# Performance work log

Measured on AMD Instinct MI355X. Metric: run time of the kernel, lower is better.

## Reference

```python
import jax, jax.numpy as jnp
import numpy as np

B, S, D, H, F = 4, 1024, 1024, 16, 4096
DH = D // H
EPS = 1e-3  # keras LayerNormalization default epsilon


def _layer_norm(x, g, b):
    mu = jnp.mean(x, axis=-1, keepdims=True)
    var = jnp.mean(jnp.square(x - mu), axis=-1, keepdims=True)
    return (x - mu) * jax.lax.rsqrt(var + EPS) * g + b


def setup_inputs() -> dict:
    key = jax.random.key(0)
    ks = jax.random.split(key, 12)
    p = lambda k, shape: (0.02 * jax.random.normal(k, shape, dtype=jnp.float32))
    inp = {
        "inputs": jax.random.normal(ks[0], (B, S, D), dtype=jnp.float32),
        "paddings": jnp.zeros((B, S), dtype=jnp.float32),
        "attention_bias": jax.random.normal(ks[1], (B, H, S, S), dtype=jnp.float32),
        "attention_mask": jnp.ones((B, S, S), dtype=jnp.float32),
        "ln1_g": jnp.ones((D,), jnp.float32), "ln1_b": jnp.zeros((D,), jnp.float32),
        "wq": p(ks[2], (D, D)), "bq": jnp.zeros((D,), jnp.float32),
        "wk": p(ks[3], (D, D)), "bk": jnp.zeros((D,), jnp.float32),
        "wv": p(ks[4], (D, D)), "bv": jnp.zeros((D,), jnp.float32),
        "wo": p(ks[5], (D, D)), "bo": jnp.zeros((D,), jnp.float32),
        "ln2_g": jnp.ones((D,), jnp.float32), "ln2_b": jnp.zeros((D,), jnp.float32),
        "w1": p(ks[6], (D, F)), "b1": jnp.zeros((F,), jnp.float32),
        "w2": p(ks[7], (F, D)), "b2": jnp.zeros((D,), jnp.float32),
    }
    return inp


def reference(inputs, paddings, attention_bias, attention_mask,
              ln1_g, ln1_b, wq, bq, wk, bk, wv, bv, wo, bo,
              ln2_g, ln2_b, w1, b1, w2, b2):
    # ----- combined mask: [B,S,S] (broadcast over heads) -----
    keep = 1.0 - paddings                           # [B,S]
    pad_mask = keep[:, :, None] * keep[:, None, :]  # [B,T,S]
    mask = attention_mask * pad_mask                # [B,T,S]

    # ----- self-attention on pre-normalized inputs -----
    xn = _layer_norm(inputs, ln1_g, ln1_b)          # [B,S,D]
    q = (xn @ wq + bq).reshape(B, S, H, DH)
    k = (xn @ wk + bk).reshape(B, S, H, DH)
    v = (xn @ wv + bv).reshape(B, S, H, DH)

    logits = jnp.einsum('bthd,bshd->bhts', q, k) / jnp.sqrt(jnp.float32(DH))
    logits = logits + attention_bias - 1e9 * (1.0 - mask[:, None, :, :])
    attn = jax.nn.softmax(logits, axis=-1)          # [B,H,T,S]
    ctx = jnp.einsum('bhts,bshd->bthd', attn, v).reshape(B, S, D)
    atten_out = ctx @ wo + bo + inputs              # residual

    # ----- feed-forward block -----
    yn = _layer_norm(atten_out, ln2_g, ln2_b)
    h = jax.nn.gelu(yn @ w1 + b1, approximate=False)  # keras 'gelu' is exact
    out = atten_out + (h @ w2 + b2)
    out = out * (1.0 - paddings[:, :, None])
    return out
```

## Files before the change

kernel.cpp:

```cpp
#include <hip/hip_runtime.h>
#include <cstdint>
#include <cstddef>

#define B_   4
#define S_   1024
#define D_   1024
#define H_   16
#define DH_  64
#define F_   4096
#define MTOT 4096
#define QKV3 3072
#define KOFF 1024
#define VOFF 2048
#define SMBASE 16.0f

typedef __bf16 bf16x8 __attribute__((ext_vector_type(8)));
typedef float  f32x4  __attribute__((ext_vector_type(4)));

__device__ __forceinline__ unsigned short f2bf(float f){
  uint32_t u = __builtin_bit_cast(uint32_t, f);
  u += 0x7fffu + ((u >> 16) & 1u);
  return (unsigned short)(u >> 16);
}

__device__ __forceinline__ void gload_lds16(const void* g, void* l){
  __builtin_amdgcn_global_load_lds((__attribute__((address_space(1))) void*)(g),
                                   (__attribute__((address_space(3))) void*)(l),
                                   16, 0, 0);
}

__global__ __launch_bounds__(256) void prep_weights(const float* __restrict__ wq,
                                                    const float* __restrict__ wk,
                                                    const float* __restrict__ wv,
                                                    const float* __restrict__ wo,
                                                    const float* __restrict__ w1,
                                                    const float* __restrict__ w2,
                                                    const float* __restrict__ bq,
                                                    const float* __restrict__ bk,
                                                    const float* __restrict__ bv,
                                                    unsigned short* __restrict__ wqkvT,
                                                    unsigned short* __restrict__ woT,
                                                    unsigned short* __restrict__ w1T,
                                                    unsigned short* __restrict__ w2T,
                                                    float* __restrict__ bqkv){
  __shared__ float tile[32][33];
  const int bid = blockIdx.x;
  const int tx = threadIdx.x, ty = threadIdx.y;
  const float* W; unsigned short* WT; int K, N, n0, k0;
  if (bid < 3072){
    W  = (bid < 1024) ? wq : (bid < 2048) ? wk : wv;
    WT = wqkvT + (size_t)(bid >> 10) * D_ * D_;
    K = D_; N = D_;
    const int t = bid & 1023; n0 = (t & 31) * 32; k0 = (t >> 5) * 32;
  } else if (bid < 4096){
    W = wo; WT = woT; K = D_; N = D_;
    const int t = bid - 3072; n0 = (t & 31) * 32; k0 = (t >> 5) * 32;
  } else if (bid < 8192){
    W = w1; WT = w1T; K = D_; N = F_;
    const int t = bid - 4096; n0 = (t & 127) * 32; k0 = (t >> 7) * 32;
  } else {
    W = w2; WT = w2T; K = F_; N = D_;
    const int t = bid - 8192; n0 = (t & 31) * 32; k0 = (t >> 5) * 32;
  }
  #pragma unroll
  for (int i = 0; i < 4; ++i)
    tile[ty + i*8][tx] = W[(size_t)(k0 + ty + i*8) * N + n0 + tx];
  __syncthreads();
  #pragma unroll
  for (int i = 0; i < 4; ++i)
    WT[(size_t)(n0 + ty + i*8) * K + k0 + tx] = f2bf(tile[tx][ty + i*8]);
  if (bid < 12){
    const int i = bid*256 + ty*32 + tx;
    bqkv[i] = (i < 1024) ? bq[i] : (i < 2048) ? bk[i - 1024] : bv[i - 2048];
  }
}

__global__ __launch_bounds__(256) void vtrans(const unsigned short* __restrict__ qkv,
                                              unsigned short* __restrict__ vt){
  __shared__ unsigned short tile[32][33];
  const int tx = threadIdx.x, ty = threadIdx.y;
  const int bid = blockIdx.x;
  const int s0 = (bid & 31) * 32;
  const int d0 = ((bid >> 5) & 1) * 32;
  const int bh = bid >> 6;
  const int b = bh >> 4, hh = bh & 15;
  #pragma unroll
  for (int i = 0; i < 4; ++i)
    tile[ty + i*8][tx] = qkv[(size_t)(b*S_ + s0 + ty + i*8) * QKV3 + VOFF + hh*DH_ + d0 + tx];
  __syncthreads();
  #pragma unroll
  for (int i = 0; i < 4; ++i)
    vt[((size_t)bh*DH_ + d0 + ty + i*8) * S_ + s0 + tx] = tile[tx][ty + i*8];
}

__global__ __launch_bounds__(256) void ln_kernel(const float* __restrict__ x,
                                                 const float* __restrict__ g,
                                                 const float* __restrict__ b,
                                                 unsigned short* __restrict__ out){
  const int row = blockIdx.x;
  const int tid = threadIdx.x;
  float4 xv = ((const float4*)(x + (size_t)row * D_))[tid];
  float s  = xv.x + xv.y + xv.z + xv.w;
  float s2 = xv.x*xv.x + xv.y*xv.y + xv.z*xv.z + xv.w*xv.w;
  #pragma unroll
  for (int off = 32; off > 0; off >>= 1){
    s  += __shfl_down(s, off);
    s2 += __shfl_down(s2, off);
  }
  __shared__ float ws1[4], ws2[4];
  const int w = tid >> 6, lane = tid & 63;
  if (lane == 0){ ws1[w] = s; ws2[w] = s2; }
  __syncthreads();
  const float tot  = ws1[0] + ws1[1] + ws1[2] + ws1[3];
  const float tot2 = ws2[0] + ws2[1] + ws2[2] + ws2[3];
  const float mean = tot * (1.0f / D_);
  const float var  = tot2 * (1.0f / D_) - mean * mean;
  const float rstd = rsqrtf(var + 1e-3f);
  const int c0 = tid * 4;
  ushort4 o;
  o.x = f2bf((xv.x - mean) * rstd * g[c0+0] + b[c0+0]);
  o.y = f2bf((xv.y - mean) * rstd * g[c0+1] + b[c0+1]);
  o.z = f2bf((xv.z - mean) * rstd * g[c0+2] + b[c0+2]);
  o.w = f2bf((xv.w - mean) * rstd * g[c0+3] + b[c0+3]);
  *(ushort4*)(out + (size_t)row * D_ + c0) = o;
}

template<int EPI, int BM>
__global__ __launch_bounds__(256) void gemm_bt(const unsigned short* __restrict__ A,
                                               const unsigned short* __restrict__ BT,
                                               const float* __restrict__ bias,
                                               const float* __restrict__ resid,
                                               const float* __restrict__ pad,
                                               unsigned short* __restrict__ outB,
                                               float* __restrict__ outF,
                                               int N, int K){
  constexpr int MR = BM / 32;
  constexpr int RA = BM / 32;
  __shared__ unsigned short As[BM * 64];
  __shared__ unsigned short Bs[128 * 64];
  const int tid  = threadIdx.x;
  const int lane = tid & 63, w = tid >> 6;
  const int wr = w >> 1, wc = w & 1;
  const int lm = lane & 15, l4 = lane >> 4;
  const int xsw = (lm & 7) << 3;
  const int m0 = blockIdx.x * BM, n0 = blockIdx.y * 128;

  const int rrow = tid >> 3;
  const int ce   = (((tid & 7) ^ (rrow & 7)) << 3);
  const unsigned short* Asrc = A  + (size_t)(m0 + rrow) * K + ce;
  const unsigned short* Bsrc = BT + (size_t)(n0 + rrow) * K + ce;

  f32x4 acc[MR][4] = {};

  #pragma unroll
  for (int ra = 0; ra < RA; ++ra)
    gload_lds16(Asrc + (size_t)(ra*32) * K, &As[(ra*256 + w*64) * 8]);
  #pragma unroll
  for (int rb = 0; rb < 4; ++rb)
    gload_lds16(Bsrc + (size_t)(rb*32) * K, &Bs[(rb*256 + w*64) * 8]);

  for (int k0 = 0; k0 < K; k0 += 64){
    __syncthreads();

    bf16x8 a[MR][2], bb[4][2];
    #pragma unroll
    for (int m = 0; m < MR; ++m)
      #pragma unroll
      for (int kc = 0; kc < 2; ++kc)
        a[m][kc] = *(const bf16x8*)&As[(wr*(BM/2) + m*16 + lm)*64 + ((kc*32 + l4*8) ^ xsw)];
    #pragma unroll
    for (int n = 0; n < 4; ++n)
      #pragma unroll
      for (int kc = 0; kc < 2; ++kc)
        bb[n][kc] = *(const bf16x8*)&Bs[(wc*64 + n*16 + lm)*64 + ((kc*32 + l4*8) ^ xsw)];

    __syncthreads();

    if (k0 + 64 < K){
      #pragma unroll
      for (int ra = 0; ra < RA; ++ra)
        gload_lds16(Asrc + (size_t)(ra*32) * K + (k0 + 64), &As[(ra*256 + w*64) * 8]);
      #pragma unroll
      for (int rb = 0; rb < 4; ++rb)
        gload_lds16(Bsrc + (size_t)(rb*32) * K + (k0 + 64), &Bs[(rb*256 + w*64) * 8]);
    }

    #pragma unroll
    for (int m = 0; m < MR; ++m)
      #pragma unroll
      for (int n = 0; n < 4; ++n)
        #pragma unroll
        for (int kc = 0; kc < 2; ++kc)
          acc[m][n] = __builtin_amdgcn_mfma_f32_16x16x32_bf16(a[m][kc], bb[n][kc], acc[m][n], 0, 0, 0);
  }

  #pragma unroll
  for (int m = 0; m < MR; ++m){
    #pragma unroll
    for (int n = 0; n < 4; ++n){
      #pragma unroll
      for (int r = 0; r < 4; ++r){
        const int row = m0 + wr*(BM/2) + m*16 + l4*4 + r;
        const int col = n0 + wc*64 + n*16 + lm;
        const size_t idx = (size_t)row * N + col;
        float vv = acc[m][n][r] + bias[col];
        if constexpr (EPI == 0){
          outB[idx] = f2bf(vv);
        } else if constexpr (EPI == 1){
          outF[idx] = vv + resid[idx];
        } else if constexpr (EPI == 2){
          outB[idx] = f2bf(0.5f * vv * (1.0f + erff(vv * 0.70710678118654752f)));
        } else {
          float t = vv + resid[idx];
          outF[idx] = t * (1.0f - pad[row]);
        }
      }
    }
  }
}

__global__ __launch_bounds__(256) void attn_kernel(const unsigned short* __restrict__ qkv,
                                                   const unsigned short* __restrict__ vt,
                                                   const float* __restrict__ abias,
                                                   const float* __restrict__ amask,
                                                   const float* __restrict__ pad,
                                                   unsigned short* __restrict__ ctx){
  const int bid = blockIdx.x;
  const int id2 = (bid & 7) * 128 + (bid >> 3);
  const int tt = id2 & 15, h = (id2 >> 4) & 15, b = id2 >> 8;
  const int t0 = tt * 64;
  const int tid = threadIdx.x;
  const int lane = tid & 63, w = tid >> 6;
  const int lm = lane & 15, l4 = lane >> 4;
  const int xsw = (lm & 7) << 3;

  __shared__ unsigned short Ks[2][64 * 64];
  __shared__ unsigned short VTs[2][64 * 64];
  __shared__ unsigned short Ps[4][16 * 64];

  bf16x8 aq[2];
  {
    const int tg = t0 + w*16 + lm;
    const size_t qb = (size_t)(b*S_ + tg) * QKV3 + h*DH_;
    aq[0] = *(const bf16x8*)&qkv[qb + 0  + l4*8];
    aq[1] = *(const bf16x8*)&qkv[qb + 32 + l4*8];
  }

  const unsigned short* kbase = qkv + (size_t)(b*S_) * QKV3 + KOFF + h*DH_;
  const unsigned short* vbase = vt  + (size_t)((b*H_ + h) * DH_) * S_;
  const float* biasbase  = abias + (size_t)((b*H_ + h) * S_ + t0 + w*16 + l4*4) * S_;
  const float* amaskbase = amask + (size_t)(b*S_ + t0 + w*16 + l4*4) * S_;
  const float* padb = pad + b*S_;

  const int r_st  = tid >> 3;
  const int ce_st = (((tid & 7) ^ (r_st & 7)) << 3);
  const unsigned short* kst = kbase + (size_t)r_st * QKV3 + ce_st;
  const unsigned short* vst = vbase + (size_t)r_st * S_ + ce_st;

  float kt[4];
  #pragma unroll
  for (int r = 0; r < 4; ++r)
    kt[r] = 1.0f - padb[t0 + w*16 + l4*4 + r];

  f32x4 accO[4] = {};
  float lrow[4] = {};
  float bmA[4][4], bmB[4][4];
  float mmA[4][4], mmB[4][4];
  float ksA[4],    ksB[4];

  auto stageKV = [&](int s0, int buf){
    gload_lds16(kst + (size_t)s0*QKV3,        &Ks[buf][w*512]);
    gload_lds16(kst + (size_t)(s0 + 32)*QKV3, &Ks[buf][2048 + w*512]);
    gload_lds16(vst + s0,                     &VTs[buf][w*512]);
    gload_lds16(vst + 32*S_ + s0,             &VTs[buf][2048 + w*512]);
  };
  auto fetchScal = [&](int s0, float (&bm)[4][4], float (&mm)[4][4], float (&ks)[4]){
    #pragma unroll
    for (int n = 0; n < 4; ++n){
      const int sg = s0 + n*16 + lm;
      ks[n] = 1.0f - padb[sg];
      #pragma unroll
      for (int r = 0; r < 4; ++r){
        bm[n][r] = biasbase[(size_t)r * S_ + sg];
        mm[n][r] = amaskbase[(size_t)r * S_ + sg];
      }
    }
  };

  stageKV(0, 0);
  fetchScal(0, bmA, mmA, ksA);

  auto step = [&](int s0, int buf, float (&bm)[4][4], float (&mm)[4][4], float (&ks)[4],
                  float (&bmN)[4][4], float (&mmN)[4][4], float (&ksN)[4]){
    __syncthreads();

    const int s1 = s0 + 64;
    if (s1 < S_){
      stageKV(s1, buf^1);
      fetchScal(s1, bmN, mmN, ksN);
    }

    f32x4 accS[4] = {};
    __builtin_amdgcn_s_setprio(1);
    #pragma unroll
    for (int n = 0; n < 4; ++n)
      #pragma unroll
      for (int kc = 0; kc < 2; ++kc){
        bf16x8 bk_ = *(const bf16x8*)&Ks[buf][(n*16 + lm)*64 + ((kc*32 + l4*8) ^ xsw)];
        accS[n] = __builtin_amdgcn_mfma_f32_16x16x32_bf16(aq[kc], bk_, accS[n], 0, 0, 0);
      }
    __builtin_amdgcn_s_setprio(0);

    float ps[4] = {};
    #pragma unroll
    for (int n = 0; n < 4; ++n){
      #pragma unroll
      for (int r = 0; r < 4; ++r){
        const float mmv = mm[n][r] * kt[r] * ks[n];
        const float ma  = -1e9f * (1.0f - mmv);
        const float pv  = __expf(fmaf(accS[n][r], 0.125f, bm[n][r] + ma) - SMBASE);
        accS[n][r] = pv;
        ps[r] += pv;
      }
    }
    #pragma unroll
    for (int r = 0; r < 4; ++r){
      float s = ps[r];
      s += __shfl_xor(s, 1); s += __shfl_xor(s, 2);
      s += __shfl_xor(s, 4); s += __shfl_xor(s, 8);
      lrow[r] += s;
    }

    #pragma unroll
    for (int n = 0; n < 4; ++n)
      #pragma unroll
      for (int r = 0; r < 4; ++r){
        const int prow = l4*4 + r;
        Ps[w][prow*64 + ((n*16 + lm) ^ ((prow & 7) << 3))] = f2bf(accS[n][r]);
      }

    __builtin_amdgcn_s_setprio(1);
    #pragma unroll
    for (int ks2 = 0; ks2 < 2; ++ks2){
      bf16x8 ap = *(const bf16x8*)&Ps[w][lm*64 + ((ks2*32 + l4*8) ^ xsw)];
      #pragma unroll
      for (int n = 0; n < 4; ++n){
        bf16x8 bv_ = *(const bf16x8*)&VTs[buf][(n*16 + lm)*64 + ((ks2*32 + l4*8) ^ xsw)];
        accO[n] = __builtin_amdgcn_mfma_f32_16x16x32_bf16(ap, bv_, accO[n], 0, 0, 0);
      }
    }
    __builtin_amdgcn_s_setprio(0);
  };

  #pragma unroll 1
  for (int s0 = 0; s0 < S_; s0 += 128){
    step(s0,      0, bmA, mmA, ksA, bmB, mmB, ksB);
    step(s0 + 64, 1, bmB, mmB, ksB, bmA, mmA, ksA);
  }

  #pragma unroll
  for (int n = 0; n < 4; ++n)
    #pragma unroll
    for (int r = 0; r < 4; ++r){
      const int tg = t0 + w*16 + l4*4 + r;
      ctx[(size_t)(b*S_ + tg) * D_ + h*DH_ + n*16 + lm] = f2bf(accO[n][r] / lrow[r]);
    }
}

extern "C" void kernel_launch(void* const* d_in, const int* in_sizes, int n_in,
                              void* d_out, int out_size, void* d_ws, size_t ws_size,
                              hipStream_t stream){
  (void)in_sizes; (void)n_in; (void)out_size; (void)ws_size;
  const float* x     = (const float*)d_in[0];
  const float* pad   = (const float*)d_in[1];
  const float* abias = (const float*)d_in[2];
  const float* amask = (const float*)d_in[3];
  const float* ln1g  = (const float*)d_in[4];
  const float* ln1b  = (const float*)d_in[5];
  const float* wq    = (const float*)d_in[6];
  const float* bq    = (const float*)d_in[7];
  const float* wk    = (const float*)d_in[8];
  const float* bk    = (const float*)d_in[9];
  const float* wv    = (const float*)d_in[10];
  const float* bv    = (const float*)d_in[11];
  const float* wo    = (const float*)d_in[12];
  const float* bo    = (const float*)d_in[13];
  const float* ln2g  = (const float*)d_in[14];
  const float* ln2b  = (const float*)d_in[15];
  const float* w1    = (const float*)d_in[16];
  const float* b1    = (const float*)d_in[17];
  const float* w2    = (const float*)d_in[18];
  const float* b2    = (const float*)d_in[19];
  float* out = (float*)d_out;

  char* p = (char*)d_ws;
  auto take = [&](size_t bytes){ void* r = (void*)p; p += bytes; return r; };
  unsigned short* xn   = (unsigned short*)take((size_t)MTOT * D_ * 2);
  unsigned short* qkv  = (unsigned short*)take((size_t)MTOT * QKV3 * 2);
  unsigned short* ctx  = (unsigned short*)take((size_t)MTOT * D_ * 2);
  unsigned short* yn   = (unsigned short*)take((size_t)MTOT * D_ * 2);
  unsigned short* hb   = (unsigned short*)take((size_t)MTOT * F_ * 2);
  float*          ao   = (float*)take((size_t)MTOT * D_ * 4);
  unsigned short* wqkvT= (unsigned short*)take((size_t)QKV3 * D_ * 2);
  unsigned short* woT  = (unsigned short*)take((size_t)D_ * D_ * 2);
  unsigned short* w1T  = (unsigned short*)take((size_t)D_ * F_ * 2);
  unsigned short* w2T  = (unsigned short*)take((size_t)D_ * F_ * 2);
  float*          bqkv = (float*)take((size_t)QKV3 * 4);
  unsigned short* vtb  = xn;

  const dim3 tb(32, 8);

  prep_weights<<<12288, tb, 0, stream>>>(wq, wk, wv, wo, w1, w2, bq, bk, bv,
                                         wqkvT, woT, w1T, w2T, bqkv);

  ln_kernel<<<MTOT, 256, 0, stream>>>(x, ln1g, ln1b, xn);

  gemm_bt<0,128><<<dim3(MTOT/128, QKV3/128), 256, 0, stream>>>(xn, wqkvT, bqkv, nullptr, nullptr, qkv, nullptr, QKV3, D_);

  vtrans<<<4096, tb, 0, stream>>>(qkv, vtb);

  attn_kernel<<<dim3(16*H_*B_), 256, 0, stream>>>(qkv, vtb, abias, amask, pad, ctx);

  gemm_bt<1,64><<<dim3(MTOT/64, D_/128), 256, 0, stream>>>(ctx, woT, bo, x, nullptr, nullptr, ao, D_, D_);

  ln_kernel<<<MTOT, 256, 0, stream>>>(ao, ln2g, ln2b, yn);

  gemm_bt<2,128><<<dim3(MTOT/128, F_/128), 256, 0, stream>>>(yn, w1T, b1, nullptr, nullptr, hb, nullptr, F_, D_);

  gemm_bt<3,64><<<dim3(MTOT/64, D_/128), 256, 0, stream>>>(hb, w2T, b2, ao, pad, nullptr, out, D_, F_);
}
```

Measured before the change: 306.6 us.

## Add 256x256-tile 8-wave GEMM with interleaved LDS staging for QKV and FFN1

Adds a new 512-thread GEMM kernel with 256x256 output tiles, double-buffered LDS split into k-halves, and a ping-pong schedule that interleaves async global-to-LDS loads with MFMA blocks separated by barriers and priority hints. The QKV projection and the first FFN GEMM now use it instead of the 128-tile kernel. The larger tile raises arithmetic intensity and data reuse per block, and the interleaving hides load latency. In exchange, the grid gets smaller (192 and 256 blocks) and register pressure rises from the 8x4 accumulator array.

```diff
diff --git a/kernel.cpp b/kernel.cpp
--- a/kernel.cpp
+++ b/kernel.cpp
@@ -219,6 +219,145 @@
   }
 }
 
+template<int EPI>
+__global__ __launch_bounds__(512, 2) void gemm8(const unsigned short* __restrict__ A,
+                                                const unsigned short* __restrict__ BT,
+                                                const float* __restrict__ bias,
+                                                unsigned short* __restrict__ outB,
+                                                int N, int K){
+  __shared__ unsigned short As[2][2][256 * 32];
+  __shared__ unsigned short Bs[2][2][256 * 32];
+  const int tid  = threadIdx.x;
+  const int lane = tid & 63, w = tid >> 6;
+  const int wr = w >> 2, wn = w & 3;
+  const int lm = lane & 15, l4 = lane >> 4;
+  const int m0 = blockIdx.x * 256, n0 = blockIdx.y * 256;
+  const int nt = K >> 6;
+
+  const int p_line = tid >> 3, p_c = tid & 7;
+  const int cp     = p_c ^ (p_line & 7);
+  const int st_row = (p_line << 1) + (cp >> 2);
+  const int st_col = (cp & 3) << 3;
+  const unsigned short* Asrc0 = A  + (size_t)(m0 + st_row)       * K + st_col;
+  const unsigned short* Asrc1 = A  + (size_t)(m0 + st_row + 128) * K + st_col;
+  const unsigned short* Bsrc0 = BT + (size_t)(n0 + st_row)       * K + st_col;
+  const unsigned short* Bsrc1 = BT + (size_t)(n0 + st_row + 128) * K + st_col;
+
+  const int arow = wr*128 + lm;
+  const int brow = wn*64  + lm;
+  const int a_off = (arow >> 1)*64 + (((((arow & 1) << 2) | l4) ^ ((arow >> 1) & 7)) << 3);
+  const int b_off = (brow >> 1)*64 + (((((brow & 1) << 2) | l4) ^ ((brow >> 1) & 7)) << 3);
+
+  f32x4 acc[8][4] = {};
+
+  auto stgA = [&](int t, int kc){
+    const int par = t & 1;
+    const size_t ko = (size_t)(t*64 + kc*32);
+    gload_lds16(Asrc0 + ko, (void*)&As[par][kc][tid*8]);
+    gload_lds16(Asrc1 + ko, (void*)&As[par][kc][4096 + tid*8]);
+  };
+  auto stgB = [&](int t, int kc){
+    const int par = t & 1;
+    const size_t ko = (size_t)(t*64 + kc*32);
+    gload_lds16(Bsrc0 + ko, (void*)&Bs[par][kc][tid*8]);
+    gload_lds16(Bsrc1 + ko, (void*)&Bs[par][kc][4096 + tid*8]);
+  };
+
+  stgA(0, 0); stgB(0, 0); stgA(0, 1); stgB(0, 1);
+  asm volatile("s_waitcnt vmcnt(4)" ::: "memory");
+  __builtin_amdgcn_s_barrier();
+
+  for (int t = 0; t < nt; ++t){
+    const int par = t & 1;
+    const int tn  = (t + 1 < nt) ? (t + 1) : 0;
+    bf16x8 a[8], b0, b1, b2, b3;
+
+    #pragma unroll
+    for (int mf = 0; mf < 8; ++mf)
+      a[mf] = *(const bf16x8*)&As[par][0][a_off + mf*512];
+    b0 = *(const bf16x8*)&Bs[par][0][b_off];
+    b1 = *(const bf16x8*)&Bs[par][0][b_off + 512];
+    stgA(tn, 0);
+    __builtin_amdgcn_s_barrier();
+    asm volatile("s_waitcnt lgkmcnt(0)" ::: "memory");
+    __builtin_amdgcn_sched_barrier(0);
+    __builtin_amdgcn_s_setprio(1);
+    #pragma unroll
+    for (int mf = 0; mf < 8; ++mf){
+      acc[mf][0] = __builtin_amdgcn_mfma_f32_16x16x32_bf16(a[mf], b0, acc[mf][0], 0, 0, 0);
+      acc[mf][1] = __builtin_amdgcn_mfma_f32_16x16x32_bf16(a[mf], b1, acc[mf][1], 0, 0, 0);
+    }
+    __builtin_amdgcn_s_setprio(0);
+    __builtin_amdgcn_s_barrier();
+
+    b2 = *(const bf16x8*)&Bs[par][0][b_off + 1024];
+    b3 = *(const bf16x8*)&Bs[par][0][b_off + 1536];
+    stgB(tn, 0);
+    __builtin_amdgcn_s_barrier();
+    asm volatile("s_waitcnt lgkmcnt(0)" ::: "memory");
+    __builtin_amdgcn_sched_barrier(0);
+    __builtin_amdgcn_s_setprio(1);
+    #pragma unroll
+    for (int mf = 0; mf < 8; ++mf){
+      acc[mf][2] = __builtin_amdgcn_mfma_f32_16x16x32_bf16(a[mf], b2, acc[mf][2], 0, 0, 0);
+      acc[mf][3] = __builtin_amdgcn_mfma_f32_16x16x32_bf16(a[mf], b3, acc[mf][3], 0, 0, 0);
+    }
+    __builtin_amdgcn_s_setprio(0);
+    asm volatile("s_waitcnt vmcnt(4)" ::: "memory");
+    __builtin_amdgcn_s_barrier();
+
+    #pragma unroll
+    for (int mf = 0; mf < 8; ++mf)
+      a[mf] = *(const bf16x8*)&As[par][1][a_off + mf*512];
+    b0 = *(const bf16x8*)&Bs[par][1][b_off];
+    b1 = *(const bf16x8*)&Bs[par][1][b_off + 512];
+    stgA(tn, 1);
+    __builtin_amdgcn_s_barrier();
+    asm volatile("s_waitcnt lgkmcnt(0)" ::: "memory");
+    __builtin_amdgcn_sched_barrier(0);
+    __builtin_amdgcn_s_setprio(1);
+    #pragma unroll
+    for (int mf = 0; mf < 8; ++mf){
+      acc[mf][0] = __builtin_amdgcn_mfma_f32_16x16x32_bf16(a[mf], b0, acc[mf][0], 0, 0, 0);
+      acc[mf][1] = __builtin_amdgcn_mfma_f32_16x16x32_bf16(a[mf], b1, acc[mf][1], 0, 0, 0);
+    }
+    __builtin_amdgcn_s_setprio(0);
+    __builtin_amdgcn_s_barrier();
+
+    b2 = *(const bf16x8*)&Bs[par][1][b_off + 1024];
+    b3 = *(const bf16x8*)&Bs[par][1][b_off + 1536];
+    stgB(tn, 1);
+    __builtin_amdgcn_s_barrier();
+    asm volatile("s_waitcnt lgkmcnt(0)" ::: "memory");
+    __builtin_amdgcn_sched_barrier(0);
+    __builtin_amdgcn_s_setprio(1);
+    #pragma unroll
+    for (int mf = 0; mf < 8; ++mf){
+      acc[mf][2] = __builtin_amdgcn_mfma_f32_16x16x32_bf16(a[mf], b2, acc[mf][2], 0, 0, 0);
+      acc[mf][3] = __builtin_amdgcn_mfma_f32_16x16x32_bf16(a[mf], b3, acc[mf][3], 0, 0, 0);
+    }
+    __builtin_amdgcn_s_setprio(0);
+    asm volatile("s_waitcnt vmcnt(4)" ::: "memory");
+    __builtin_amdgcn_s_barrier();
+  }
+
+  #pragma unroll
+  for (int mf = 0; mf < 8; ++mf){
+    #pragma unroll
+    for (int nf = 0; nf < 4; ++nf){
+      #pragma unroll
+      for (int r = 0; r < 4; ++r){
+        const int row = m0 + wr*128 + mf*16 + l4*4 + r;
+        const int col = n0 + wn*64 + nf*16 + lm;
+        float vv = acc[mf][nf][r] + bias[col];
+        if constexpr (EPI == 2)
+          vv = 0.5f * vv * (1.0f + erff(vv * 0.70710678118654752f));
+        outB[(size_t)row * N + col] = f2bf(vv);
+      }
+    }
+  }
+}
+
 __global__ __launch_bounds__(256) void attn_kernel(const unsigned short* __restrict__ qkv,
                                                    const unsigned short* __restrict__ vt,
                                                    const float* __restrict__ abias,
@@ -415,7 +554,7 @@
 
   ln_kernel<<<MTOT, 256, 0, stream>>>(x, ln1g, ln1b, xn);
 
-  gemm_bt<0,128><<<dim3(MTOT/128, QKV3/128), 256, 0, stream>>>(xn, wqkvT, bqkv, nullptr, nullptr, qkv, nullptr, QKV3, D_);
+  gemm8<0><<<dim3(MTOT/256, QKV3/256), 512, 0, stream>>>(xn, wqkvT, bqkv, qkv, QKV3, D_);
 
   vtrans<<<4096, tb, 0, stream>>>(qkv, vtb);
 
@@ -425,7 +564,7 @@
 
   ln_kernel<<<MTOT, 256, 0, stream>>>(ao, ln2g, ln2b, yn);
 
-  gemm_bt<2,128><<<dim3(MTOT/128, F_/128), 256, 0, stream>>>(yn, w1T, b1, nullptr, nullptr, hb, nullptr, F_, D_);
+  gemm8<2><<<dim3(MTOT/256, F_/256), 512, 0, stream>>>(yn, w1T, b1, hb, F_, D_);
 
   gemm_bt<3,64><<<dim3(MTOT/64, D_/128), 256, 0, stream>>>(hb, w2T, b2, ao, pad, nullptr, out, D_, F_);
 }
```

Result: slower. 356.5 us (+16.2%).
